# Kernel optimization log

Hardware: AMD Instinct MI355X
Metric: run time of the kernel (lower is better)

The kernel has to match this reference:

```python
import jax, jax.numpy as jnp
import numpy as np

K = 512
D = 256


def setup_inputs() -> dict:
    key = jax.random.key(0)
    k1, k2 = jax.random.split(key)
    z_e = jax.random.normal(k1, (64, D, 32, 32), dtype=jnp.float32)
    # torch init: uniform_(-1/K, 1/K)
    codebook = jax.random.uniform(k2, (K, D), dtype=jnp.float32, minval=-1.0 / K, maxval=1.0 / K)
    return {"z_e": z_e, "codebook": codebook}


def reference(z_e, codebook):
    B, C, H, W = z_e.shape
    # (B,C,H,W) -> (B,H,W,C) -> (N,D)
    z_flat = jnp.transpose(z_e, (0, 2, 3, 1)).reshape(-1, C)
    # squared L2 distances: ||z||^2 + ||e||^2 - 2 z.e  -> [N, K]
    d = (jnp.sum(z_flat ** 2, axis=1, keepdims=True)
         + jnp.sum(codebook ** 2, axis=1)
         - 2.0 * jnp.matmul(z_flat, codebook.T))
    idx = jnp.argmin(d, axis=1)  # [N]
    z_q_flat = codebook[idx]  # [N, D] gather
    z_q = jnp.transpose(z_q_flat.reshape(B, H, W, C), (0, 3, 1, 2))
    commitment_loss = jnp.mean((z_e - jax.lax.stop_gradient(z_q)) ** 2)
    codebook_loss = jnp.mean((z_q - jax.lax.stop_gradient(z_e)) ** 2)
    # straight-through estimator
    z_q_st = z_e + jax.lax.stop_gradient(z_q - z_e)
    indices = idx.reshape(B, H, W)
    return (z_q_st, commitment_loss, codebook_loss, indices)
```

## Files before the change

kernel.cpp:

```cpp
#include <hip/hip_runtime.h>


typedef __attribute__((ext_vector_type(8))) short short8v;
typedef __attribute__((ext_vector_type(4))) float float4v;
typedef unsigned short ushort_t;

#define GLOAD_LDS16(gsrc, ldst)                                                \
    __builtin_amdgcn_global_load_lds(                                          \
        (const __attribute__((address_space(1))) unsigned*)(gsrc),             \
        (__attribute__((address_space(3))) unsigned*)(ldst), 16, 0, 0)

namespace {
constexpr int K = 512;
constexpr int D = 256;
constexpr int HW = 1024;
constexpr int NROWS = 65536;
constexpr int CHW = D * HW;

constexpr int ZQ_SIZE = 64 * CHW;
constexpr int LOSS0_OFF = ZQ_SIZE;
constexpr int LOSS1_OFF = ZQ_SIZE + 1;
constexpr int IDX_OFF = ZQ_SIZE + 2;

constexpr int WS_EH_FLOATS = (K * D) / 2;
constexpr int WS_B = WS_EH_FLOATS;
constexpr int WS_KIDX = WS_B + K;
constexpr int WS_PART = WS_KIDX + NROWS;

constexpr int NBLK_A = NROWS / 32;
constexpr int NBLK_G = 2048;

constexpr float EPS_CAND = 3.0e-3f;
constexpr int MAXC = 16;
}

__device__ __forceinline__ ushort_t bf16_rne(float f) {
    unsigned u = __float_as_uint(f);
    u += 0x7fffu + ((u >> 16) & 1u);
    return (ushort_t)(u >> 16);
}

__global__ void vq_prep(const float* __restrict__ cb, float* __restrict__ ws) {
    const int k = blockIdx.x;
    const int t = threadIdx.x;
    ushort_t* ehb = (ushort_t*)ws;
    {
        const int s = t >> 5;
        const int kg = (t >> 3) & 3;
        const int j = t & 7;
        ehb[(size_t)((s * 4 + kg) * 512 + k) * 8 + j] = bf16_rne(cb[k * D + t]);
    }
    __shared__ float r16[16];
    if (t < 16) {
#pragma clang fp contract(off)
        const float* x = cb + k * D + (t >> 3) * 128;
        const int j = t & 7;
        float v = x[j];
        float r = v * v;
        for (int i = 1; i < 16; ++i) {
            float w = x[8 * i + j];
            r += w * w;
        }
        r16[t] = r;
    }
    __syncthreads();
    if (t == 0) {
#pragma clang fp contract(off)
        float lo = ((r16[0] + r16[1]) + (r16[2] + r16[3])) +
                   ((r16[4] + r16[5]) + (r16[6] + r16[7]));
        float hi = ((r16[8] + r16[9]) + (r16[10] + r16[11])) +
                   ((r16[12] + r16[13]) + (r16[14] + r16[15]));
        ws[WS_B + k] = lo + hi;
    }
}

__global__ __launch_bounds__(256, 2) void vq_argmin4(
    const float* __restrict__ z_e, const float* __restrict__ cb,
    const ushort_t* __restrict__ ehb, const float* __restrict__ Bv,
    int* __restrict__ wsidx, float* __restrict__ out) {
    __shared__ __align__(16) ushort_t elds[4][512][8];
    __shared__ __align__(16) ushort_t zh[32][264];
    __shared__ float lds_B[K];
    __shared__ float scr[32][17];
    __shared__ int cand[32][MAXC];
    __shared__ float lds_A[32];
    __shared__ float wmin[4][32];
    __shared__ float rmin[32];
    __shared__ int cnt[32];

    const int t = threadIdx.x;
    const int row0 = blockIdx.x * 32;
    const int b = row0 >> 10;
    const int hw0 = row0 & 1023;
    const float* zbase = z_e + (size_t)b * CHW + hw0;

    lds_B[t] = Bv[t];
    lds_B[t + 256] = Bv[t + 256];

    {
        const int row = t & 31;
        const int q = t >> 5;
        const int half = q >> 2;
        const int j0 = (q & 3) * 2;
        const int cbase = half * 128;
        const float* zp = zbase + row;
        float za0[16], za1[16];
#pragma unroll
        for (int i = 0; i < 16; ++i) {
            const int c = cbase + 8 * i + j0;
            za0[i] = zp[(size_t)c * HW];
            za1[i] = zp[(size_t)(c + 1) * HW];
        }
        float r0, r1;
        {
#pragma clang fp contract(off)
            r0 = za0[0] * za0[0];
            r1 = za1[0] * za1[0];
#pragma unroll
            for (int i = 1; i < 16; ++i) {
                r0 += za0[i] * za0[i];
                r1 += za1[i] * za1[i];
            }
        }
#pragma unroll
        for (int i = 0; i < 16; ++i) {
            const int c = cbase + 8 * i + j0;
            *reinterpret_cast<unsigned*>(&zh[row][c]) =
                (unsigned)bf16_rne(za0[i]) | ((unsigned)bf16_rne(za1[i]) << 16);
        }
        scr[row][half * 8 + j0] = r0;
        scr[row][half * 8 + j0 + 1] = r1;
    }
    __syncthreads();
    if (t < 32) {
#pragma clang fp contract(off)
        const float* r = scr[t];
        float lo = ((r[0] + r[1]) + (r[2] + r[3])) + ((r[4] + r[5]) + (r[6] + r[7]));
        float hi = ((r[8] + r[9]) + (r[10] + r[11])) + ((r[12] + r[13]) + (r[14] + r[15]));
        lds_A[t] = lo + hi;
    }

    const int lane = t & 63;
    const int w = t >> 6;
    const int wc0 = w * 128;
    const int l15 = lane & 15;
    const int kg = lane >> 4;

    float4v acc[8][2];
#pragma unroll
    for (int c = 0; c < 8; ++c)
#pragma unroll
        for (int rt = 0; rt < 2; ++rt) acc[c][rt] = (float4v)0.f;

    const char* gtile = (const char*)ehb + (size_t)w * 8192 + (size_t)lane * 16;
    char* ltile = (char*)&elds[w][0][0];

    for (int s = 0; s < 8; ++s) {
        const char* gs = gtile + (size_t)s * 32768;
#pragma unroll
        for (int i = 0; i < 8; ++i) GLOAD_LDS16(gs + i * 1024, ltile + i * 1024);
        asm volatile("s_waitcnt vmcnt(0)" ::: "memory");
        __syncthreads();

        const int d0 = s * 32;
        const short8v bh0 = *reinterpret_cast<const short8v*>(&zh[l15][d0 + 8 * kg]);
        const short8v bh1 = *reinterpret_cast<const short8v*>(&zh[16 + l15][d0 + 8 * kg]);
#pragma unroll
        for (int c = 0; c < 8; ++c) {
            const short8v a =
                *reinterpret_cast<const short8v*>(&elds[kg][wc0 + c * 16 + l15][0]);
            acc[c][0] = __builtin_amdgcn_mfma_f32_16x16x32_bf16(a, bh0, acc[c][0], 0, 0, 0);
            acc[c][1] = __builtin_amdgcn_mfma_f32_16x16x32_bf16(a, bh1, acc[c][1], 0, 0, 0);
        }
        __syncthreads();
    }

    float lmin0 = 3.0e38f, lmin1 = 3.0e38f;
#pragma unroll
    for (int c = 0; c < 8; ++c)
#pragma unroll
        for (int rt = 0; rt < 2; ++rt)
#pragma unroll
            for (int r = 0; r < 4; ++r) {
                const int code = wc0 + 16 * c + 4 * kg + r;
                const int row = rt * 16 + l15;
                float s = (lds_A[row] + lds_B[code]) - 2.0f * acc[c][rt][r];
                acc[c][rt][r] = s;
                if (rt == 0) lmin0 = fminf(lmin0, s);
                else lmin1 = fminf(lmin1, s);
            }
    lmin0 = fminf(lmin0, __shfl_xor(lmin0, 16));
    lmin0 = fminf(lmin0, __shfl_xor(lmin0, 32));
    lmin1 = fminf(lmin1, __shfl_xor(lmin1, 16));
    lmin1 = fminf(lmin1, __shfl_xor(lmin1, 32));
    if (lane < 16) {
        wmin[w][l15] = lmin0;
        wmin[w][16 + l15] = lmin1;
    }
    __syncthreads();
    if (t < 32) {
        rmin[t] = fminf(fminf(wmin[0][t], wmin[1][t]), fminf(wmin[2][t], wmin[3][t]));
        cnt[t] = 0;
    }
    __syncthreads();

#pragma unroll
    for (int c = 0; c < 8; ++c)
#pragma unroll
        for (int rt = 0; rt < 2; ++rt) {
            const int row = rt * 16 + l15;
            const float thr = rmin[row] + EPS_CAND;
#pragma unroll
            for (int r = 0; r < 4; ++r) {
                if (acc[c][rt][r] <= thr) {
                    const int code = wc0 + 16 * c + 4 * kg + r;
                    int slot = atomicAdd(&cnt[row], 1);
                    if (slot < MAXC) cand[row][slot] = code;
                }
            }
        }
    __syncthreads();

    float* ed = reinterpret_cast<float*>(&zh[0][0]);
    int* ek = reinterpret_cast<int*>(ed + 256);
    {
        const int row = t & 31;
        const int ct = t >> 5;
        const float* zp = zbase + row;
        const int n = cnt[row];
        float bd = 3.0e38f;
        int bk = 0x7fffffff;
        if (n == 1) {
            if (ct == 0) {
                bd = -3.0e38f;
                bk = cand[row][0];
            }
        } else {
            const bool full = (n > MAXC);
            const int lim = full ? K : n;
            for (int s = ct; s < lim; s += 8) {
                const int k = full ? s : cand[row][s];
                const float* ep = cb + (size_t)k * D;
                float a = 0.f;
#pragma unroll 8
                for (int c = 0; c < D; ++c) a = fmaf(zp[(size_t)c * HW], ep[c], a);
                float dv;
                {
#pragma clang fp contract(off)
                    float t1 = lds_A[row] + lds_B[k];
                    dv = t1 - 2.0f * a;
                }
                if (dv < bd || (dv == bd && k < bk)) {
                    bd = dv;
                    bk = k;
                }
            }
        }
        ed[t] = bd;
        ek[t] = bk;
    }
    __syncthreads();
    if (t < 32) {
        float bd = ed[t];
        int bk = ek[t];
#pragma unroll
        for (int q = 1; q < 8; ++q) {
            float od = ed[q * 32 + t];
            int ok = ek[q * 32 + t];
            if (od < bd || (od == bd && ok < bk)) {
                bd = od;
                bk = ok;
            }
        }
        wsidx[row0 + t] = bk;
        out[IDX_OFF + row0 + t] = (float)bk;
    }
}

__global__ __launch_bounds__(256, 8) void vq_gather2(
    const float* __restrict__ z_e, const float* __restrict__ cb,
    const int* __restrict__ wsidx, float* __restrict__ part,
    float* __restrict__ out) {
    __shared__ float wpart[4];
    const int t = threadIdx.x;
    const int blk = blockIdx.x;
    const int cg = blk & 7;
    const int q = (blk >> 3) & 3;
    const int b = blk >> 5;
    const int lane = t & 63;
    const int csub = t >> 6;
    const int hw = q * 256 + lane * 4;

    const int4 kk = *reinterpret_cast<const int4*>(&wsidx[b * HW + hw]);
    const float* e0 = cb + (size_t)kk.x * D;
    const float* e1 = cb + (size_t)kk.y * D;
    const float* e2 = cb + (size_t)kk.z * D;
    const float* e3 = cb + (size_t)kk.w * D;
    const size_t zoff = (size_t)b * CHW + hw;

    float accum = 0.f;
#pragma unroll 2
    for (int i = 0; i < 8; ++i) {
        const int c = cg * 32 + csub * 8 + i;
        const size_t off = zoff + (size_t)c * HW;
        const float4 z4 = *reinterpret_cast<const float4*>(&z_e[off]);
        const float ex = e0[c], ey = e1[c], ez = e2[c], ew = e3[c];
        float4 o4;
        o4.x = z4.x + (ex - z4.x);
        o4.y = z4.y + (ey - z4.y);
        o4.z = z4.z + (ez - z4.z);
        o4.w = z4.w + (ew - z4.w);
        *reinterpret_cast<float4*>(&out[off]) = o4;
        accum = fmaf(z4.x - ex, z4.x - ex, accum);
        accum = fmaf(z4.y - ey, z4.y - ey, accum);
        accum = fmaf(z4.z - ez, z4.z - ez, accum);
        accum = fmaf(z4.w - ew, z4.w - ew, accum);
    }
#pragma unroll
    for (int m = 1; m < 64; m <<= 1) accum += __shfl_xor(accum, m);
    if (lane == 0) wpart[csub] = accum;
    __syncthreads();
    if (t == 0) part[blk] = (wpart[0] + wpart[1]) + (wpart[2] + wpart[3]);
}

__global__ void vq_finish(const float* __restrict__ part, float* __restrict__ out) {
    const int t = threadIdx.x;
    double s = 0.0;
#pragma unroll
    for (int i = 0; i < 8; ++i) s += (double)part[t + 256 * i];
#pragma unroll
    for (int m = 1; m < 64; m <<= 1) s += __shfl_xor(s, m);
    __shared__ double wsum[4];
    if ((t & 63) == 0) wsum[t >> 6] = s;
    __syncthreads();
    if (t == 0) {
        double mean = (wsum[0] + wsum[1] + wsum[2] + wsum[3]) / (double)ZQ_SIZE;
        out[LOSS0_OFF] = (float)mean;
        out[LOSS1_OFF] = (float)mean;
    }
}

extern "C" void kernel_launch(void* const* d_in, const int* in_sizes, int n_in,
                              void* d_out, int out_size, void* d_ws, size_t ws_size,
                              hipStream_t stream) {
    const float* z_e = (const float*)d_in[0];
    const float* cb = (const float*)d_in[1];
    float* out = (float*)d_out;
    float* ws = (float*)d_ws;

    const ushort_t* ehb = (const ushort_t*)ws;
    float* Bv = ws + WS_B;
    int* wsidx = (int*)(ws + WS_KIDX);
    float* part = ws + WS_PART;

    vq_prep<<<K, D, 0, stream>>>(cb, ws);
    vq_argmin4<<<NBLK_A, 256, 0, stream>>>(z_e, cb, ehb, Bv, wsidx, out);
    vq_gather2<<<NBLK_G, 256, 0, stream>>>(z_e, cb, wsidx, part, out);
    vq_finish<<<1, 256, 0, stream>>>(part, out);
}
```

Measured before the change: 131.3 us.

## Stage fp32 z tile in LDS via async global-to-LDS loads, convert to bf16 per step

The argmin kernel now copies the block's 32-row by 256-channel fp32 z tile into shared memory with global_load_lds DMA, replacing the per-thread strided global loads and the separate bf16 z buffer. Row norms, MFMA B-operand conversion (bf16 rounding done inside the k-loop while codebook loads are in flight) and the fp32 candidate rescoring all read z from LDS rather than re-reading global memory. This is meant to cut strided global traffic, especially during rescoring. In exchange it uses more LDS (32KB fp32 tile instead of about 17KB bf16), which may limit occupancy, and it adds per-step conversion work plus possible LDS bank conflicts on column reads.

```diff
diff --git a/kernel.cpp b/kernel.cpp
--- a/kernel.cpp
+++ b/kernel.cpp
@@ -74,12 +74,12 @@
     }
 }
 
-__global__ __launch_bounds__(256, 2) void vq_argmin4(
+__global__ __launch_bounds__(256, 2) void vq_argmin5(
     const float* __restrict__ z_e, const float* __restrict__ cb,
     const ushort_t* __restrict__ ehb, const float* __restrict__ Bv,
     int* __restrict__ wsidx, float* __restrict__ out) {
+    __shared__ __align__(16) float zf[256][32];
     __shared__ __align__(16) ushort_t elds[4][512][8];
-    __shared__ __align__(16) ushort_t zh[32][264];
     __shared__ float lds_B[K];
     __shared__ float scr[32][17];
     __shared__ int cand[32][MAXC];
@@ -89,13 +89,27 @@
     __shared__ int cnt[32];
 
     const int t = threadIdx.x;
+    const int lane = t & 63;
+    const int w = t >> 6;
     const int row0 = blockIdx.x * 32;
     const int b = row0 >> 10;
     const int hw0 = row0 & 1023;
     const float* zbase = z_e + (size_t)b * CHW + hw0;
 
+    {
+        const char* zg = (const char*)zbase;
+        char* zl = (char*)&zf[0][0];
+#pragma unroll
+        for (int i = 0; i < 8; ++i) {
+            const int cc = (w * 8 + i) * 8 + (lane >> 3);
+            GLOAD_LDS16(zg + (size_t)cc * 4096 + (lane & 7) * 16,
+                        zl + (size_t)(w * 8 + i) * 1024);
+        }
+    }
     lds_B[t] = Bv[t];
     lds_B[t + 256] = Bv[t + 256];
+    asm volatile("s_waitcnt vmcnt(0)" ::: "memory");
+    __syncthreads();
 
     {
         const int row = t & 31;
@@ -103,30 +117,20 @@
         const int half = q >> 2;
         const int j0 = (q & 3) * 2;
         const int cbase = half * 128;
-        const float* zp = zbase + row;
-        float za0[16], za1[16];
-#pragma unroll
-        for (int i = 0; i < 16; ++i) {
-            const int c = cbase + 8 * i + j0;
-            za0[i] = zp[(size_t)c * HW];
-            za1[i] = zp[(size_t)(c + 1) * HW];
-        }
         float r0, r1;
         {
 #pragma clang fp contract(off)
-            r0 = za0[0] * za0[0];
-            r1 = za1[0] * za1[0];
+            float w0 = zf[cbase + j0][row];
+            float w1 = zf[cbase + j0 + 1][row];
+            r0 = w0 * w0;
+            r1 = w1 * w1;
 #pragma unroll
             for (int i = 1; i < 16; ++i) {
-                r0 += za0[i] * za0[i];
-                r1 += za1[i] * za1[i];
-            }
-        }
-#pragma unroll
-        for (int i = 0; i < 16; ++i) {
-            const int c = cbase + 8 * i + j0;
-            *reinterpret_cast<unsigned*>(&zh[row][c]) =
-                (unsigned)bf16_rne(za0[i]) | ((unsigned)bf16_rne(za1[i]) << 16);
+                float u0 = zf[cbase + 8 * i + j0][row];
+                float u1 = zf[cbase + 8 * i + j0 + 1][row];
+                r0 += u0 * u0;
+                r1 += u1 * u1;
+            }
         }
         scr[row][half * 8 + j0] = r0;
         scr[row][half * 8 + j0 + 1] = r1;
@@ -140,8 +144,6 @@
         lds_A[t] = lo + hi;
     }
 
-    const int lane = t & 63;
-    const int w = t >> 6;
     const int wc0 = w * 128;
     const int l15 = lane & 15;
     const int kg = lane >> 4;
@@ -159,12 +161,18 @@
         const char* gs = gtile + (size_t)s * 32768;
 #pragma unroll
         for (int i = 0; i < 8; ++i) GLOAD_LDS16(gs + i * 1024, ltile + i * 1024);
+
+        const int d0 = s * 32;
+        short8v bh0, bh1;
+#pragma unroll
+        for (int j = 0; j < 8; ++j) {
+            bh0[j] = (short)bf16_rne(zf[d0 + 8 * kg + j][l15]);
+            bh1[j] = (short)bf16_rne(zf[d0 + 8 * kg + j][16 + l15]);
+        }
+
         asm volatile("s_waitcnt vmcnt(0)" ::: "memory");
         __syncthreads();
 
-        const int d0 = s * 32;
-        const short8v bh0 = *reinterpret_cast<const short8v*>(&zh[l15][d0 + 8 * kg]);
-        const short8v bh1 = *reinterpret_cast<const short8v*>(&zh[16 + l15][d0 + 8 * kg]);
 #pragma unroll
         for (int c = 0; c < 8; ++c) {
             const short8v a =
@@ -221,12 +229,11 @@
         }
     __syncthreads();
 
-    float* ed = reinterpret_cast<float*>(&zh[0][0]);
+    float* ed = reinterpret_cast<float*>(&elds[0][0][0]);
     int* ek = reinterpret_cast<int*>(ed + 256);
     {
         const int row = t & 31;
         const int ct = t >> 5;
-        const float* zp = zbase + row;
         const int n = cnt[row];
         float bd = 3.0e38f;
         int bk = 0x7fffffff;
@@ -243,7 +250,7 @@
                 const float* ep = cb + (size_t)k * D;
                 float a = 0.f;
 #pragma unroll 8
-                for (int c = 0; c < D; ++c) a = fmaf(zp[(size_t)c * HW], ep[c], a);
+                for (int c = 0; c < D; ++c) a = fmaf(zf[c][row], ep[c], a);
                 float dv;
                 {
 #pragma clang fp contract(off)
@@ -354,7 +361,7 @@
     float* part = ws + WS_PART;
 
     vq_prep<<<K, D, 0, stream>>>(cb, ws);
-    vq_argmin4<<<NBLK_A, 256, 0, stream>>>(z_e, cb, ehb, Bv, wsidx, out);
+    vq_argmin5<<<NBLK_A, 256, 0, stream>>>(z_e, cb, ehb, Bv, wsidx, out);
     vq_gather2<<<NBLK_G, 256, 0, stream>>>(z_e, cb, wsidx, part, out);
     vq_finish<<<1, 256, 0, stream>>>(part, out);
 }
```

New measurement: 121.2 us. 1.08x faster.
